# Kernel tuning notes

Measured on AMD Instinct MI355X. Metric: run time of the kernel, lower is better.

Reference implementation:

```python
import jax, jax.numpy as jnp
import numpy as np

N_EMITTERS = 200000
N_FRAMES = 500


def setup_inputs() -> dict:
    key = jax.random.key(0)
    k1, _ = jax.random.split(key)
    # initial state must be one-hot per emitter: column 0 = 'on', column 1 = 'off'
    on = jax.random.bernoulli(k1, 0.5, (N_EMITTERS,))
    initial = jnp.stack([on, ~on], axis=-1).astype(jnp.float32)  # [N, 2] one-hot
    # transition[j] is the categorical distribution over {stay-ish, flip-ish} given row j
    transition = jnp.array([[0.5, 0.5], [0.9, 0.1]], dtype=jnp.float32)
    # transition_matrix[0] = identity (keep state), transition_matrix[1] = swap (flip state)
    transition_matrix = jnp.array([[[1.0, 0.0], [0.0, 1.0]],
                                   [[0.0, 1.0], [1.0, 0.0]]], dtype=jnp.float32)
    return {"initial": initial, "transition": transition,
            "transition_matrix": transition_matrix, "n_frames": N_FRAMES}


def reference(initial, transition, transition_matrix, n_frames):
    # Faithful translation of the per-frame Python loop as a single lax.scan.
    # Original: A = Cat(transition).sample([N]) -> A[n, j] ~ Cat(transition[j, :]) in {0, 1}
    #           t = (state * A).sum(-1)   (selects A at the current one-hot state index)
    #           state = state @ transition_matrix[t]
    # Output: per-frame on-mask (original returned np.where(state[:, 0] == 1) indices,
    # which has data-dependent shape; we return the equivalent dense mask).
    p1 = transition[:, 1]  # prob of drawing class 1 for each of the 2 row-distributions
    keys = jax.random.split(jax.random.key(42), n_frames)

    def step(state, k):
        u = jax.random.uniform(k, (state.shape[0], 2), dtype=state.dtype)  # [N, 2]
        A = (u < p1[None, :]).astype(state.dtype)  # categorical sample per row dist, {0,1}
        t = jnp.sum(state * A, axis=-1).astype(jnp.int32)  # [N] chosen action per emitter
        m = transition_matrix[t]  # [N, 2, 2] identity-or-swap
        new_state = jnp.einsum('ni,nij->nj', state, m)  # [N, 2] one-hot update
        return new_state, new_state[:, 0]

    _, on_mask = jax.lax.scan(step, initial, keys)
    return on_mask  # [n_frames, N], 1.0 where emitter is in the 'on' state
```

## Files before the change

kernel.cpp:

```cpp
#include <hip/hip_runtime.h>
#include <stdint.h>


#define ROTL32(x, d) __builtin_rotateleft32((x), (d))

__device__ __forceinline__ void tf2x32(uint32_t k0, uint32_t k1,
                                       uint32_t x0, uint32_t x1,
                                       uint32_t& o0, uint32_t& o1) {
  const uint32_t k2 = k0 ^ k1 ^ 0x1BD11BDAu;
  x0 += k0; x1 += k1;
#define TF_R(d) { x0 += x1; x1 = ROTL32(x1, d) ^ x0; }
  TF_R(13) TF_R(15) TF_R(26) TF_R(6)
  x0 += k1; x1 += k2 + 1u;
  TF_R(17) TF_R(29) TF_R(16) TF_R(24)
  x0 += k2; x1 += k0 + 2u;
  TF_R(13) TF_R(15) TF_R(26) TF_R(6)
  x0 += k0; x1 += k1 + 3u;
  TF_R(17) TF_R(29) TF_R(16) TF_R(24)
  x0 += k1; x1 += k2 + 4u;
  TF_R(13) TF_R(15) TF_R(26) TF_R(6)
  x0 += k2; x1 += k0 + 5u;
#undef TF_R
  o0 = x0; o1 = x1;
}

template <int NCH>
__device__ __forceinline__ void frames_loop(
    const uint2* __restrict__ kf, int nf, int N,
    uint32_t base0, uint32_t base1, int s0, int s1,
    uint32_t thr0, uint32_t thr1, int sw0, int sw1,
    float* __restrict__ o0, float* __restrict__ o1) {
  uint2 ck = kf[0];
  for (int f = 0; f < nf; ++f) {
    const uint32_t k0 = ck.x, k1 = ck.y;
    ck = kf[f + 1];
    const uint32_t k2 = k0 ^ k1 ^ 0x1BD11BDAu;
    const uint32_t c1 = k2 + 1u, c2 = k0 + 2u, c3 = k1 + 3u,
                   c4 = k2 + 4u, c5 = k0 + 5u;

    const uint32_t ta_thr = (s0 != 0) ? thr1 : thr0;
    const uint32_t tb_thr = (s1 != 0) ? thr1 : thr0;

    uint32_t xa0 = k0, xa1 = base0 + (uint32_t)s0 + k1;
    uint32_t xb0 = k0, xb1 = base1 + (uint32_t)s1 + k1;

#define RND(d)                                             \
  { xa0 += xa1; xa1 = ROTL32(xa1, (d)) ^ xa0;              \
    if (NCH == 2) { xb0 += xb1; xb1 = ROTL32(xb1, (d)) ^ xb0; } }
#define INJ(ia, ib)                                        \
  { xa0 += (ia); xa1 += (ib);                              \
    if (NCH == 2) { xb0 += (ia); xb1 += (ib); } }

    RND(13) RND(15) RND(26) RND(6)
    INJ(k1, c1)
    RND(17) RND(29) RND(16) RND(24)
    INJ(k2, c2)
    RND(13) RND(15) RND(26) RND(6)
    INJ(k0, c3)
    RND(17) RND(29) RND(16) RND(24)
    INJ(k1, c4)
    RND(13) RND(15) RND(26) RND(6)
    INJ(k2, c5)
#undef RND
#undef INJ

    const int ta = (((xa0 ^ xa1) >> 9) < ta_thr) ? 1 : 0;
    s0 ^= ta ? sw1 : sw0;
    *o0 = (s0 == 0) ? 1.0f : 0.0f;
    o0 += N;
    if (NCH == 2) {
      const int tb = (((xb0 ^ xb1) >> 9) < tb_thr) ? 1 : 0;
      s1 ^= tb ? sw1 : sw0;
      *o1 = (s1 == 0) ? 1.0f : 0.0f;
      o1 += N;
    }
  }
}

__global__ __launch_bounds__(256) void markov_kernel(
    const float* __restrict__ initial, const float* __restrict__ transition,
    const float* __restrict__ tmat, float* __restrict__ out,
    int N, int nf, int T) {
  extern __shared__ uint2 kf[];
  for (int f = threadIdx.x; f <= nf; f += blockDim.x) {
    uint2 k = make_uint2(0u, 0u);
    if (f < nf) {
      uint32_t a, b;
      tf2x32(0u, 42u, 0u, (uint32_t)f, a, b);
      k = make_uint2(a, b);
    }
    kf[f] = k;
  }
  __syncthreads();

  const int t = blockIdx.x * blockDim.x + threadIdx.x;
  if (t >= N) return;

  const uint32_t thr0 = (uint32_t)ceilf(transition[1] * 8388608.0f);
  const uint32_t thr1 = (uint32_t)ceilf(transition[3] * 8388608.0f);
  const int sw0 = (tmat[1] != 0.0f) ? 1 : 0;
  const int sw1 = (tmat[5] != 0.0f) ? 1 : 0;

  const int n0 = t;
  const int n1 = t + T;
  const int s0 = (initial[2 * n0] != 0.0f) ? 0 : 1;

  if (n1 < N) {
    const int s1 = (initial[2 * n1] != 0.0f) ? 0 : 1;
    frames_loop<2>(kf, nf, N, (uint32_t)(2 * n0), (uint32_t)(2 * n1), s0, s1,
                   thr0, thr1, sw0, sw1, out + n0, out + n1);
  } else {
    frames_loop<1>(kf, nf, N, (uint32_t)(2 * n0), 0u, s0, 0,
                   thr0, thr1, sw0, sw1, out + n0, out + n0);
  }
}

extern "C" void kernel_launch(void* const* d_in, const int* in_sizes, int n_in,
                              void* d_out, int out_size, void* d_ws, size_t ws_size,
                              hipStream_t stream) {
  const float* initial    = (const float*)d_in[0];
  const float* transition = (const float*)d_in[1];
  const float* tmat       = (const float*)d_in[2];
  float* out = (float*)d_out;

  const int N  = in_sizes[0] / 2;
  const int nf = (N > 0) ? (out_size / N) : 0;
  if (N <= 0 || nf <= 0) return;

  int T;
  if (N >= 131072) T = 131072;
  else T = ((N + 255) / 256) * 256;

  const int block = 256;
  const int grid = T / block;
  const size_t shmem = (size_t)(nf + 1) * sizeof(uint2);
  hipLaunchKernelGGL(markov_kernel, dim3(grid), dim3(block), shmem, stream,
                     initial, transition, tmat, out, N, nf, T);
}
```

Before: 281.4 us.

## Precompute subkeys in separate kernel and rebalance emitter split across 64-thread blocks

Per-frame subkeys now come from a small separate kernel that writes them into workspace, so the main kernel no longer fills shared memory in every block. The main kernel reads them from global memory instead. Emitters are split evenly in half (each thread handles tid and tid+ceil(N/2)) with 64-thread blocks, which removes the uneven single-chain tail threads and produces more blocks. The random-number threshold is pre-shifted so the per-frame >>9 is dropped, and the next frame's threshold is selected right after each state update. The cost is an extra launch and global-memory key reads in place of LDS reads.

```diff
diff --git a/kernel.cpp b/kernel.cpp
--- a/kernel.cpp
+++ b/kernel.cpp
@@ -24,63 +24,99 @@
   o0 = x0; o1 = x1;
 }
 
-template <int NCH>
-__device__ __forceinline__ void frames_loop(
-    const uint2* __restrict__ kf, int nf, int N,
-    uint32_t base0, uint32_t base1, int s0, int s1,
-    uint32_t thr0, uint32_t thr1, int sw0, int sw1,
-    float* __restrict__ o0, float* __restrict__ o1) {
-  uint2 ck = kf[0];
+__global__ void subkeys_kernel(uint2* __restrict__ ks, int nf) {
+  const int f = blockIdx.x * blockDim.x + threadIdx.x;
+  if (f < nf) {
+    uint32_t a, b;
+    tf2x32(0u, 42u, 0u, (uint32_t)f, a, b);
+    ks[f] = make_uint2(a, b);
+  } else if (f == nf) {
+    ks[f] = make_uint2(0u, 0u);
+  }
+}
+
+__device__ __forceinline__ void run_dual(
+    const uint2* __restrict__ ks, int nf, int N,
+    int nA, int nB, bool hasB, uint32_t sA, uint32_t sB,
+    uint32_t tsh0, uint32_t tsh1, uint32_t sw0, uint32_t sw1,
+    float* __restrict__ out) {
+  uint32_t thrA = sA ? tsh1 : tsh0;
+  uint32_t thrB = sB ? tsh1 : tsh0;
+  const uint32_t baseA = 2u * (uint32_t)nA;
+  const uint32_t baseB = 2u * (uint32_t)nB;
+
+  float* op = out;
+  uint2 ck = ks[0];
   for (int f = 0; f < nf; ++f) {
     const uint32_t k0 = ck.x, k1 = ck.y;
-    ck = kf[f + 1];
+    ck = ks[f + 1];
     const uint32_t k2 = k0 ^ k1 ^ 0x1BD11BDAu;
     const uint32_t c1 = k2 + 1u, c2 = k0 + 2u, c3 = k1 + 3u,
                    c4 = k2 + 4u, c5 = k0 + 5u;
 
-    const uint32_t ta_thr = (s0 != 0) ? thr1 : thr0;
-    const uint32_t tb_thr = (s1 != 0) ? thr1 : thr0;
+    uint32_t xa0 = k0, xa1 = baseA + sA + k1;
+    uint32_t xb0 = k0, xb1 = baseB + sB + k1;
 
-    uint32_t xa0 = k0, xa1 = base0 + (uint32_t)s0 + k1;
-    uint32_t xb0 = k0, xb1 = base1 + (uint32_t)s1 + k1;
+#define RND(d) { xa0 += xa1; xa1 = ROTL32(xa1, (d)) ^ xa0;   \
+                 xb0 += xb1; xb1 = ROTL32(xb1, (d)) ^ xb0; }
+    RND(13) RND(15) RND(26) RND(6)
+    xa0 += k1; xa1 += c1; xb0 += k1; xb1 += c1;
+    RND(17) RND(29) RND(16) RND(24)
+    xa0 += k2; xa1 += c2; xb0 += k2; xb1 += c2;
+    RND(13) RND(15) RND(26) RND(6)
+    xa0 += k0; xa1 += c3; xb0 += k0; xb1 += c3;
+    RND(17) RND(29) RND(16) RND(24)
+    xa0 += k1; xa1 += c4; xb0 += k1; xb1 += c4;
+    RND(13) RND(15) RND(26) RND(6)
+    xa0 += k2; xa1 += c5; xb0 += k2; xb1 += c5;
+#undef RND
 
-#define RND(d)                                             \
-  { xa0 += xa1; xa1 = ROTL32(xa1, (d)) ^ xa0;              \
-    if (NCH == 2) { xb0 += xb1; xb1 = ROTL32(xb1, (d)) ^ xb0; } }
-#define INJ(ia, ib)                                        \
-  { xa0 += (ia); xa1 += (ib);                              \
-    if (NCH == 2) { xb0 += (ia); xb1 += (ib); } }
-
-    RND(13) RND(15) RND(26) RND(6)
-    INJ(k1, c1)
-    RND(17) RND(29) RND(16) RND(24)
-    INJ(k2, c2)
-    RND(13) RND(15) RND(26) RND(6)
-    INJ(k0, c3)
-    RND(17) RND(29) RND(16) RND(24)
-    INJ(k1, c4)
-    RND(13) RND(15) RND(26) RND(6)
-    INJ(k2, c5)
-#undef RND
-#undef INJ
-
-    const int ta = (((xa0 ^ xa1) >> 9) < ta_thr) ? 1 : 0;
-    s0 ^= ta ? sw1 : sw0;
-    *o0 = (s0 == 0) ? 1.0f : 0.0f;
-    o0 += N;
-    if (NCH == 2) {
-      const int tb = (((xb0 ^ xb1) >> 9) < tb_thr) ? 1 : 0;
-      s1 ^= tb ? sw1 : sw0;
-      *o1 = (s1 == 0) ? 1.0f : 0.0f;
-      o1 += N;
-    }
+    const uint32_t ra = xa0 ^ xa1;
+    const uint32_t rb = xb0 ^ xb1;
+    sA ^= (ra < thrA) ? sw1 : sw0;
+    sB ^= (rb < thrB) ? sw1 : sw0;
+    thrA = sA ? tsh1 : tsh0;
+    thrB = sB ? tsh1 : tsh0;
+    op[nA] = sA ? 0.0f : 1.0f;
+    if (hasB) op[nB] = sB ? 0.0f : 1.0f;
+    op += N;
   }
 }
 
-__global__ __launch_bounds__(256) void markov_kernel(
+__device__ __forceinline__ void markov_body(
+    const float* __restrict__ initial, const float* __restrict__ transition,
+    const float* __restrict__ tmat, const uint2* __restrict__ ks,
+    float* __restrict__ out, int N, int nf, int Th) {
+  const int tid = blockIdx.x * blockDim.x + threadIdx.x;
+  if (tid >= N) return;
+  const int nA = tid;
+  const int nB = tid + Th;
+  const bool hasB = (nB < N);
+
+  const uint64_t t0w = ((uint64_t)(uint32_t)ceilf(transition[1] * 8388608.0f)) << 9;
+  const uint64_t t1w = ((uint64_t)(uint32_t)ceilf(transition[3] * 8388608.0f)) << 9;
+  const uint32_t tsh0 = (t0w > 0xFFFFFFFFull) ? 0xFFFFFFFFu : (uint32_t)t0w;
+  const uint32_t tsh1 = (t1w > 0xFFFFFFFFull) ? 0xFFFFFFFFu : (uint32_t)t1w;
+  const uint32_t sw0 = (tmat[1] != 0.0f) ? 1u : 0u;
+  const uint32_t sw1 = (tmat[5] != 0.0f) ? 1u : 0u;
+
+  const uint32_t sA = (initial[2 * nA] != 0.0f) ? 0u : 1u;
+  const uint32_t sB = hasB ? ((initial[2 * nB] != 0.0f) ? 0u : 1u) : 0u;
+
+  run_dual(ks, nf, N, nA, nB, hasB, sA, sB, tsh0, tsh1, sw0, sw1, out);
+}
+
+__global__ __launch_bounds__(64) void markov_kernel(
+    const float* __restrict__ initial, const float* __restrict__ transition,
+    const float* __restrict__ tmat, const uint2* __restrict__ ks,
+    float* __restrict__ out, int N, int nf, int Th) {
+  markov_body(initial, transition, tmat, ks, out, N, nf, Th);
+}
+
+__global__ __launch_bounds__(64) void markov_kernel_lds(
     const float* __restrict__ initial, const float* __restrict__ transition,
     const float* __restrict__ tmat, float* __restrict__ out,
-    int N, int nf, int T) {
+    int N, int nf, int Th) {
   extern __shared__ uint2 kf[];
   for (int f = threadIdx.x; f <= nf; f += blockDim.x) {
     uint2 k = make_uint2(0u, 0u);
@@ -92,27 +128,7 @@
     kf[f] = k;
   }
   __syncthreads();
-
-  const int t = blockIdx.x * blockDim.x + threadIdx.x;
-  if (t >= N) return;
-
-  const uint32_t thr0 = (uint32_t)ceilf(transition[1] * 8388608.0f);
-  const uint32_t thr1 = (uint32_t)ceilf(transition[3] * 8388608.0f);
-  const int sw0 = (tmat[1] != 0.0f) ? 1 : 0;
-  const int sw1 = (tmat[5] != 0.0f) ? 1 : 0;
-
-  const int n0 = t;
-  const int n1 = t + T;
-  const int s0 = (initial[2 * n0] != 0.0f) ? 0 : 1;
-
-  if (n1 < N) {
-    const int s1 = (initial[2 * n1] != 0.0f) ? 0 : 1;
-    frames_loop<2>(kf, nf, N, (uint32_t)(2 * n0), (uint32_t)(2 * n1), s0, s1,
-                   thr0, thr1, sw0, sw1, out + n0, out + n1);
-  } else {
-    frames_loop<1>(kf, nf, N, (uint32_t)(2 * n0), 0u, s0, 0,
-                   thr0, thr1, sw0, sw1, out + n0, out + n0);
-  }
+  markov_body(initial, transition, tmat, kf, out, N, nf, Th);
 }
 
 extern "C" void kernel_launch(void* const* d_in, const int* in_sizes, int n_in,
@@ -127,13 +143,17 @@
   const int nf = (N > 0) ? (out_size / N) : 0;
   if (N <= 0 || nf <= 0) return;
 
-  int T;
-  if (N >= 131072) T = 131072;
-  else T = ((N + 255) / 256) * 256;
+  const int Th = (((N + 1) / 2) + 63) & ~63;
+  const int grid = Th / 64;
 
-  const int block = 256;
-  const int grid = T / block;
-  const size_t shmem = (size_t)(nf + 1) * sizeof(uint2);
-  hipLaunchKernelGGL(markov_kernel, dim3(grid), dim3(block), shmem, stream,
-                     initial, transition, tmat, out, N, nf, T);
+  const size_t need = (size_t)(nf + 1) * sizeof(uint2);
+  if (ws_size >= need) {
+    uint2* ks = (uint2*)d_ws;
+    subkeys_kernel<<<(nf + 1 + 255) / 256, 256, 0, stream>>>(ks, nf);
+    markov_kernel<<<grid, 64, 0, stream>>>(initial, transition, tmat, ks,
+                                           out, N, nf, Th);
+  } else {
+    markov_kernel_lds<<<grid, 64, need, stream>>>(initial, transition, tmat,
+                                                  out, N, nf, Th);
+  }
 }
```

Result: no change. 281.3 us (-0.0%).
